# Kernel tuning notes

Hardware: AMD Instinct MI355X
Metric: run time of the kernel (lower is better)

Reference implementation:

```python
import jax, jax.numpy as jnp
import numpy as np

RHO = 1.0          # ADMM penalty
LAM = 0.1          # lambda_sparse
MAX_ITERS = 20
ZETA = 0.05        # APAS drift threshold / CDS temperature
TAU = 0.1          # chiral stabilizer tolerance
STEP = 0.1         # gradient step size
COHESION = 1.0     # Mohr-Coulomb cohesion
MU = 0.5           # Mohr-Coulomb friction coefficient
DP_K = 10.0        # Drucker-Prager deviatoric-norm radius


def _pas(c):
    # Phase Alignment Invariant: scalar phase-coherence metric in [0,1]
    return jnp.abs(jnp.mean(jnp.cos(c)))


def _chirality(c):
    # odd (sign-sensitive) global moment
    return jnp.mean(c ** 3)


def _mc_proj(c, g):
    # Mohr-Coulomb yield projection: clamp magnitude to cohesion + mu*|grad|
    return jnp.sign(c) * jnp.minimum(jnp.abs(c), COHESION + MU * jnp.abs(g))


def _dp_proj(c):
    # Drucker-Prager: project deviatoric part onto norm ball of radius DP_K (per row)
    m = jnp.mean(c, axis=-1, keepdims=True)
    dev = c - m
    n = jnp.linalg.norm(dev, axis=-1, keepdims=True)
    scale = jnp.minimum(1.0, DP_K / (n + 1e-8))
    return m + dev * scale


def setup_inputs() -> dict:
    key = jax.random.key(0)
    k1, k2, k3 = jax.random.split(key, 3)
    B, D = 1024, 2048
    initial_c = 0.5 * jax.random.normal(k1, (B, D), dtype=jnp.float32)
    W = jax.random.normal(k2, (D, D), dtype=jnp.float32) / np.float32(np.sqrt(D))
    love_w = 1.0 + 0.01 * jax.random.normal(k3, (D,), dtype=jnp.float32)
    love_b = jnp.zeros((D,), dtype=jnp.float32)
    return {"initial_c": initial_c, "W": W, "love_w": love_w, "love_b": love_b}


def _forward(initial_c, W, love_w, love_b):
    c_sym = initial_c
    c0 = initial_c
    z0 = c0
    u0 = jnp.zeros_like(c0)
    prev_pas0 = _pas(c0)
    prev_score0 = -_chirality(c0)  # drift = 0 -> exp(0) = 1

    def step(carry, _):
        c, z, u, prev_pas, prev_score, low, done = carry

        def energy(ci):
            pred = ci @ W  # forward_op_fn
            violation_pressure = 0.5 * jnp.sum((pred - ci) ** 2)
            admm_tension = 0.5 * RHO * jnp.sum((ci - z + u) ** 2)
            return violation_pressure + admm_tension

        g = jax.grad(energy)(c)
        c_yield = _mc_proj(c, g)
        c_next = (c_yield * love_w + love_b) - STEP * g  # LoveVector then step
        z_in = c_next + u
        thr = LAM / RHO
        z_next = jnp.sign(z_in) * jnp.maximum(jnp.abs(z_in) - thr, 0.0)
        u_next = u + (c_next - z_next)

        cur_pas = _pas(c_next)
        drift = jnp.abs(cur_pas - prev_pas)
        violation = drift > ZETA
        low = jnp.where(cur_pas < 0.5, low + 1, 0)
        done = done | (low > 20)
        cur_score = -_chirality(c_next) * jnp.exp(-drift / ZETA)
        stable = (cur_score - prev_score) >= -TAU
        acc = (~violation) & stable & (~done)

        sel = lambda a, b: jnp.where(acc, a, b)
        new = (sel(c_next, c), sel(z_next, z), sel(u_next, u),
               jnp.where(acc, cur_pas, prev_pas),
               jnp.where(acc, cur_score, prev_score), low, done)
        return new, None

    init = (c0, z0, u0, prev_pas0, prev_score0,
            jnp.zeros((), jnp.int32), jnp.zeros((), jnp.bool_))
    (c_phys, z, u, _, _, _, _), _ = jax.lax.scan(step, init, None, length=MAX_ITERS)

    diff = jnp.linalg.norm(c_phys - c_sym)
    chi_cur = _chirality(c_phys)
    chi_orig = _chirality(c_sym)
    status = jnp.where(jnp.sign(chi_cur) != jnp.sign(chi_orig),
                       2,
                       jnp.where(diff > 5.0, 2, jnp.where(diff > 1.0, 1, 0))).astype(jnp.int32)

    delta = c_phys - c_sym
    symbolic_delta = jnp.round(delta * 10.0) / 10.0
    c_compressed = _dp_proj(c_sym + symbolic_delta)
    return c_compressed, status


def reference(initial_c, W, love_w, love_b):
    return _forward(initial_c, W, love_w, love_b)
```

## Files before the change

### kernel.cpp

```cpp
#include <hip/hip_runtime.h>
#include <math.h>

#define D 2048
#define BROWS 1024
#define NEL (D*BROWS)
#define NBLK 1024
#define NTHREADS_TOT (NBLK*256)

#define GM 128
#define GN 128
#define GK 16

__device__ __forceinline__ double blk_reduce(double v, double* sm) {
    const int t = threadIdx.x;
    sm[t] = v;
    __syncthreads();
    for (int s = 128; s > 0; s >>= 1) {
        if (t < s) sm[t] += sm[t + s];
        __syncthreads();
    }
    double r = sm[0];
    __syncthreads();
    return r;
}

__global__ __launch_bounds__(256) void k_gemm(const float* __restrict__ A,
        const float* __restrict__ B, float* __restrict__ P0, float* __restrict__ P1,
        const float* __restrict__ Wadj, int ksz, int mode, const int* __restrict__ frz)
{
    if (frz && *frz) return;
    __shared__ float As[2][GK][GM + 4];
    __shared__ float Bs[2][GK][GN + 4];
    const int t  = threadIdx.x;
    const int tx = t & 15, ty = t >> 4;
    const int row0 = blockIdx.y * GM, col0 = blockIdx.x * GN;
    const int k0 = blockIdx.z * ksz;
    float* __restrict__ out = blockIdx.z ? P1 : P0;

    const int r0 = t >> 2, cq = t & 3;

    float acc[8][8];
    #pragma unroll
    for (int i = 0; i < 8; ++i)
        #pragma unroll
        for (int j = 0; j < 8; ++j) acc[i][j] = 0.0f;

    const int ntiles = ksz / GK;
    float4 rga[2], rgb[2];

    #pragma unroll
    for (int v = 0; v < 2; ++v) {
        rga[v] = *reinterpret_cast<const float4*>(&A[(size_t)(row0 + r0 + 64*v) * D + k0 + cq*4]);
        rgb[v] = *reinterpret_cast<const float4*>(&B[(size_t)(col0 + r0 + 64*v) * D + k0 + cq*4]);
    }
    #pragma unroll
    for (int v = 0; v < 2; ++v) {
        As[0][cq*4+0][r0+64*v] = rga[v].x; As[0][cq*4+1][r0+64*v] = rga[v].y;
        As[0][cq*4+2][r0+64*v] = rga[v].z; As[0][cq*4+3][r0+64*v] = rga[v].w;
        Bs[0][cq*4+0][r0+64*v] = rgb[v].x; Bs[0][cq*4+1][r0+64*v] = rgb[v].y;
        Bs[0][cq*4+2][r0+64*v] = rgb[v].z; Bs[0][cq*4+3][r0+64*v] = rgb[v].w;
    }
    __syncthreads();

    for (int tt = 0; tt < ntiles; ++tt) {
        const int cur = tt & 1;
        if (tt + 1 < ntiles) {
            const int kb = k0 + (tt + 1) * GK;
            #pragma unroll
            for (int v = 0; v < 2; ++v) {
                rga[v] = *reinterpret_cast<const float4*>(&A[(size_t)(row0 + r0 + 64*v) * D + kb + cq*4]);
                rgb[v] = *reinterpret_cast<const float4*>(&B[(size_t)(col0 + r0 + 64*v) * D + kb + cq*4]);
            }
        }
        #pragma unroll
        for (int k = 0; k < GK; ++k) {
            float a[8], b[8];
            *reinterpret_cast<float4*>(&a[0]) = *reinterpret_cast<const float4*>(&As[cur][k][ty*4]);
            *reinterpret_cast<float4*>(&a[4]) = *reinterpret_cast<const float4*>(&As[cur][k][64 + ty*4]);
            *reinterpret_cast<float4*>(&b[0]) = *reinterpret_cast<const float4*>(&Bs[cur][k][tx*4]);
            *reinterpret_cast<float4*>(&b[4]) = *reinterpret_cast<const float4*>(&Bs[cur][k][64 + tx*4]);
            #pragma unroll
            for (int i = 0; i < 8; ++i)
                #pragma unroll
                for (int j = 0; j < 8; ++j)
                    acc[i][j] += a[i] * b[j];
        }
        if (tt + 1 < ntiles) {
            const int nb = cur ^ 1;
            __syncthreads();
            #pragma unroll
            for (int v = 0; v < 2; ++v) {
                As[nb][cq*4+0][r0+64*v] = rga[v].x; As[nb][cq*4+1][r0+64*v] = rga[v].y;
                As[nb][cq*4+2][r0+64*v] = rga[v].z; As[nb][cq*4+3][r0+64*v] = rga[v].w;
                Bs[nb][cq*4+0][r0+64*v] = rgb[v].x; Bs[nb][cq*4+1][r0+64*v] = rgb[v].y;
                Bs[nb][cq*4+2][r0+64*v] = rgb[v].z; Bs[nb][cq*4+3][r0+64*v] = rgb[v].w;
            }
            __syncthreads();
        }
    }

    #pragma unroll
    for (int i = 0; i < 8; ++i) {
        const int grow = row0 + ((i < 4) ? (ty*4 + i) : (64 + ty*4 + i - 4));
        float vv[8];
        #pragma unroll
        for (int j = 0; j < 8; ++j) vv[j] = acc[i][j];
        if (mode == 0) {
            #pragma unroll
            for (int j = 0; j < 8; ++j) {
                const int gcol = col0 + ((j < 4) ? (tx*4 + j) : (64 + tx*4 + j - 4));
                const float wsum = Wadj[(size_t)grow * D + gcol] + Wadj[(size_t)gcol * D + grow];
                vv[j] += (grow == gcol ? 1.0f : 0.0f) - wsum;
            }
        }
        float* orow = &out[(size_t)grow * D + col0];
        *reinterpret_cast<float4*>(&orow[tx*4]) =
            make_float4(vv[0], vv[1], vv[2], vv[3]);
        *reinterpret_cast<float4*>(&orow[64 + tx*4]) =
            make_float4(vv[4], vv[5], vv[6], vv[7]);
    }
}

__global__ __launch_bounds__(256) void k_init(const float* __restrict__ c0,
        float* __restrict__ c, float* __restrict__ z, float* __restrict__ u,
        double* __restrict__ partials)
{
    __shared__ double sm[256];
    double sc = 0.0, s3 = 0.0;
    const int tid = blockIdx.x * 256 + threadIdx.x;
    const float4 zero4 = make_float4(0.f, 0.f, 0.f, 0.f);
    for (int i4 = tid; i4 < NEL/4; i4 += NTHREADS_TOT) {
        const float4 v4 = reinterpret_cast<const float4*>(c0)[i4];
        reinterpret_cast<float4*>(c)[i4] = v4;
        reinterpret_cast<float4*>(z)[i4] = v4;
        reinterpret_cast<float4*>(u)[i4] = zero4;
        const float va[4] = {v4.x, v4.y, v4.z, v4.w};
        #pragma unroll
        for (int L = 0; L < 4; ++L) {
            sc += (double)cosf(va[L]);
            s3 += (double)((va[L] * va[L]) * va[L]);
        }
    }
    const double tc = blk_reduce(sc, sm);
    const double t3 = blk_reduce(s3, sm);
    if (threadIdx.x == 0) { partials[blockIdx.x] = tc; partials[NBLK + blockIdx.x] = t3; }
}

__global__ __launch_bounds__(256) void k_decide0(const double* __restrict__ partials,
        double* __restrict__ scal, int* __restrict__ flag, int* __restrict__ frz,
        int* __restrict__ sel)
{
    __shared__ double sm[256];
    const int t = threadIdx.x;
    const double a = partials[t] + partials[t+256] + partials[t+512] + partials[t+768];
    const double b = partials[NBLK+t] + partials[NBLK+t+256] + partials[NBLK+t+512] + partials[NBLK+t+768];
    const double tc = blk_reduce(a, sm);
    const double t3 = blk_reduce(b, sm);
    if (t == 0) {
        const double pas = fabs(tc / (double)NEL);
        const double chi = t3 / (double)NEL;
        scal[0] = pas; scal[1] = -chi; scal[2] = chi;
        *flag = 0; *frz = 0; *sel = 0;
    }
}

__global__ __launch_bounds__(256) void k_elem_pp(const float* __restrict__ P0,
        const float* __restrict__ P1, const float* __restrict__ cc,
        float* __restrict__ cn, float* __restrict__ z, float* __restrict__ u,
        const float* __restrict__ lw, const float* __restrict__ lb,
        double* __restrict__ partials, const int* __restrict__ frz)
{
#pragma clang fp contract(off)
    if (*frz) return;
    __shared__ double sm[256];
    double sc = 0.0, s3 = 0.0;
    const int tid = blockIdx.x * 256 + threadIdx.x;
    for (int i4 = tid; i4 < NEL/4; i4 += NTHREADS_TOT) {
        const int j4 = i4 & (D/4 - 1);
        const float4 p0 = reinterpret_cast<const float4*>(P0)[i4];
        const float4 p1 = reinterpret_cast<const float4*>(P1)[i4];
        const float4 cv4 = reinterpret_cast<const float4*>(cc)[i4];
        const float4 zv4 = reinterpret_cast<const float4*>(z)[i4];
        const float4 uv4 = reinterpret_cast<const float4*>(u)[i4];
        const float4 w4 = reinterpret_cast<const float4*>(lw)[j4];
        const float4 b4 = reinterpret_cast<const float4*>(lb)[j4];
        const float p0a[4] = {p0.x, p0.y, p0.z, p0.w};
        const float p1a[4] = {p1.x, p1.y, p1.z, p1.w};
        const float cva[4] = {cv4.x, cv4.y, cv4.z, cv4.w};
        const float zva[4] = {zv4.x, zv4.y, zv4.z, zv4.w};
        const float uva[4] = {uv4.x, uv4.y, uv4.z, uv4.w};
        const float w4a[4] = {w4.x, w4.y, w4.z, w4.w};
        const float b4a[4] = {b4.x, b4.y, b4.z, b4.w};
        float Rc[4], Rz[4], Ru[4];
        #pragma unroll
        for (int L = 0; L < 4; ++L) {
            const float cv = cva[L];
            const float uv = uva[L];
            const float g = (p0a[L] + p1a[L]) + ((cv - zva[L]) + uv);
            const float lim = 1.0f + 0.5f * fabsf(g);
            const float mn = fminf(fabsf(cv), lim);
            const float cy = (cv > 0.0f) ? mn : ((cv < 0.0f) ? -mn : 0.0f);
            const float cnv = (cy * w4a[L] + b4a[L]) - 0.1f * g;
            Rc[L] = cnv;
            const float zi = cnv + uv;
            float zm = fabsf(zi) - 0.1f;
            zm = fmaxf(zm, 0.0f);
            const float zn = (zi > 0.0f) ? zm : ((zi < 0.0f) ? -zm : 0.0f);
            Rz[L] = zn;
            Ru[L] = uv + (cnv - zn);
            sc += (double)cosf(cnv);
            s3 += (double)((cnv * cnv) * cnv);
        }
        reinterpret_cast<float4*>(cn)[i4] = make_float4(Rc[0], Rc[1], Rc[2], Rc[3]);
        reinterpret_cast<float4*>(z)[i4]  = make_float4(Rz[0], Rz[1], Rz[2], Rz[3]);
        reinterpret_cast<float4*>(u)[i4]  = make_float4(Ru[0], Ru[1], Ru[2], Ru[3]);
    }
    const double tc = blk_reduce(sc, sm);
    const double t3 = blk_reduce(s3, sm);
    if (threadIdx.x == 0) { partials[blockIdx.x] = tc; partials[NBLK + blockIdx.x] = t3; }
}

__global__ __launch_bounds__(256) void k_elem(float* __restrict__ P0,
        const float* __restrict__ P1, const float* __restrict__ c,
        const float* __restrict__ z, const float* __restrict__ u,
        const float* __restrict__ lw, const float* __restrict__ lb,
        double* __restrict__ partials, const int* __restrict__ frz)
{
#pragma clang fp contract(off)
    if (*frz) return;
    __shared__ double sm[256];
    double sc = 0.0, s3 = 0.0;
    const int tid = blockIdx.x * 256 + threadIdx.x;
    for (int i = tid; i < NEL; i += NTHREADS_TOT) {
        const int j = i & (D - 1);
        const float cv = c[i];
        const float g = (P0[i] + P1[i]) + ((cv - z[i]) + u[i]);
        const float lim = 1.0f + 0.5f * fabsf(g);
        const float mn = fminf(fabsf(cv), lim);
        const float cy = (cv > 0.0f) ? mn : ((cv < 0.0f) ? -mn : 0.0f);
        const float cnv = (cy * lw[j] + lb[j]) - 0.1f * g;
        P0[i] = cnv;
        sc += (double)cosf(cnv);
        s3 += (double)((cnv * cnv) * cnv);
    }
    const double tc = blk_reduce(sc, sm);
    const double t3 = blk_reduce(s3, sm);
    if (threadIdx.x == 0) { partials[blockIdx.x] = tc; partials[NBLK + blockIdx.x] = t3; }
}

__global__ __launch_bounds__(256) void k_decide(const double* __restrict__ partials,
        double* __restrict__ scal, int* __restrict__ flag, int* __restrict__ frz,
        int* __restrict__ sel, int next_sel)
{
    __shared__ double sm[256];
    if (*frz) return;
    const int t = threadIdx.x;
    const double a = partials[t] + partials[t+256] + partials[t+512] + partials[t+768];
    const double b = partials[NBLK+t] + partials[NBLK+t+256] + partials[NBLK+t+512] + partials[NBLK+t+768];
    const double tc = blk_reduce(a, sm);
    const double t3 = blk_reduce(b, sm);
    if (t == 0) {
        const double pas = fabs(tc / (double)NEL);
        const double drift = fabs(pas - scal[0]);
        const double chi = t3 / (double)NEL;
        const double score = -chi * exp(-drift / 0.05);
        const bool violation = drift > 0.05;
        const bool stable = (score - scal[1]) >= -0.1;
        const int acc = (!violation && stable) ? 1 : 0;
        *flag = acc;
        if (acc) { scal[0] = pas; scal[1] = score; *sel = next_sel; }
        else     { *frz = 1; }
    }
}

__global__ __launch_bounds__(256) void k_commit(const float* __restrict__ cn,
        float* __restrict__ c, float* __restrict__ z, float* __restrict__ u,
        const int* __restrict__ flag)
{
#pragma clang fp contract(off)
    if (*flag == 0) return;
    const int tid = blockIdx.x * 256 + threadIdx.x;
    for (int i = tid; i < NEL; i += NTHREADS_TOT) {
        const float cnv = cn[i];
        const float uv = u[i];
        const float zi = cnv + uv;
        float zm = fabsf(zi) - 0.1f;
        zm = fmaxf(zm, 0.0f);
        const float zn = (zi > 0.0f) ? zm : ((zi < 0.0f) ? -zm : 0.0f);
        c[i] = cnv;
        z[i] = zn;
        u[i] = uv + (cnv - zn);
    }
}

__global__ __launch_bounds__(256) void k_final_rows(const float* __restrict__ c0,
        const float* __restrict__ cA, const float* __restrict__ cB,
        const int* __restrict__ sel, float* __restrict__ outp)
{
#pragma clang fp contract(off)
    __shared__ double sm[256];
    const float* __restrict__ c = (*sel) ? cB : cA;
    const int row = blockIdx.x;
    const size_t base = (size_t)row * D;
    float tv[8];
    double s1 = 0.0;
    #pragma unroll
    for (int s = 0; s < 8; ++s) {
        const int j = threadIdx.x + s * 256;
        const float s0 = c0[base + j];
        const float delta = c[base + j] - s0;
        const float sym = rintf(delta * 10.0f) / 10.0f;
        const float tval = s0 + sym;
        tv[s] = tval;
        s1 += (double)tval;
    }
    const double tot = blk_reduce(s1, sm);
    const float m = (float)(tot / (double)D);
    double s2 = 0.0;
    #pragma unroll
    for (int s = 0; s < 8; ++s) {
        const float dev = tv[s] - m;
        s2 += (double)(dev * dev);
    }
    const double tot2 = blk_reduce(s2, sm);
    const float n = sqrtf((float)tot2);
    const float scale = fminf(1.0f, 10.0f / (n + 1e-8f));
    #pragma unroll
    for (int s = 0; s < 8; ++s) {
        const int j = threadIdx.x + s * 256;
        outp[base + j] = m + (tv[s] - m) * scale;
    }
}

__global__ __launch_bounds__(256) void k_final_glob(const float* __restrict__ c0,
        const float* __restrict__ cA, const float* __restrict__ cB,
        const int* __restrict__ sel, double* __restrict__ partials)
{
    __shared__ double sm[256];
    const float* __restrict__ c = (*sel) ? cB : cA;
    double s3 = 0.0, sd = 0.0;
    const int tid = blockIdx.x * 256 + threadIdx.x;
    for (int i = tid; i < NEL; i += NTHREADS_TOT) {
        const float v = c[i];
        s3 += (double)((v * v) * v);
        const float d = v - c0[i];
        sd += (double)(d * d);
    }
    const double t3 = blk_reduce(s3, sm);
    const double td = blk_reduce(sd, sm);
    if (threadIdx.x == 0) { partials[blockIdx.x] = t3; partials[NBLK + blockIdx.x] = td; }
}

__global__ __launch_bounds__(256) void k_final_status(const double* __restrict__ partials,
        const double* __restrict__ scal, float* __restrict__ outp)
{
    __shared__ double sm[256];
    const int t = threadIdx.x;
    const double a = partials[t] + partials[t+256] + partials[t+512] + partials[t+768];
    const double b = partials[NBLK+t] + partials[NBLK+t+256] + partials[NBLK+t+512] + partials[NBLK+t+768];
    const double t3 = blk_reduce(a, sm);
    const double td = blk_reduce(b, sm);
    if (t == 0) {
        const double chi_cur = t3 / (double)NEL;
        const double diff = sqrt(td);
        const double chi_orig = scal[2];
        const int s_cur = (chi_cur > 0.0) - (chi_cur < 0.0);
        const int s_org = (chi_orig > 0.0) - (chi_orig < 0.0);
        int status;
        if (s_cur != s_org)   status = 2;
        else if (diff > 5.0)  status = 2;
        else if (diff > 1.0)  status = 1;
        else                  status = 0;
        outp[NEL] = (float)status;
    }
}

extern "C" void kernel_launch(void* const* d_in, const int* in_sizes, int n_in,
                              void* d_out, int out_size, void* d_ws, size_t ws_size,
                              hipStream_t stream)
{
    const float* c0 = (const float*)d_in[0];
    const float* W  = (const float*)d_in[1];
    const float* lw = (const float*)d_in[2];
    const float* lb = (const float*)d_in[3];
    float* outp = (float*)d_out;

    const size_t M4 = (size_t)D * D;
    const size_t N4 = (size_t)NEL;
    float* Mb = (float*)d_ws;
    float* region = Mb + M4;

    const size_t tail_bytes = (2 * NBLK + 8) * sizeof(double) + 4 * sizeof(int);
    const bool pp = ws_size >= (M4 + 6 * N4) * sizeof(float) + tail_bytes;

    float *cA, *cB, *z, *u, *P0, *P1;
    if (pp) { cA = region; cB = cA + N4; z = cB + N4; u = z + N4; P0 = u + N4; P1 = P0 + N4; }
    else    { cA = region; cB = cA;      z = cA + N4; u = z + N4; P0 = u + N4; P1 = P0 + N4; }
    double* partials = (double*)(P1 + N4);
    double* scal = partials + 2 * NBLK;
    int* flag = (int*)(scal + 8);
    int* frz  = flag + 1;
    int* sel  = frz + 1;

    k_gemm<<<dim3(D / GN, D / GM, 1), 256, 0, stream>>>(W, W, Mb, Mb, W, D, 0, nullptr);
    k_init<<<NBLK, 256, 0, stream>>>(c0, cA, z, u, partials);
    k_decide0<<<1, 256, 0, stream>>>(partials, scal, flag, frz, sel);

    for (int t = 0; t < 20; ++t) {
        const float* ccur = (pp && (t & 1)) ? cB : cA;
        float* cnxt = (pp && !(t & 1)) ? cB : cA;
        k_gemm<<<dim3(D / GN, BROWS / GM, 2), 256, 0, stream>>>(ccur, Mb, P0, P1, nullptr, D / 2, 1, frz);
        if (pp) {
            k_elem_pp<<<NBLK, 256, 0, stream>>>(P0, P1, ccur, cnxt, z, u, lw, lb, partials, frz);
            k_decide<<<1, 256, 0, stream>>>(partials, scal, flag, frz, sel, (t + 1) & 1);
        } else {
            k_elem<<<NBLK, 256, 0, stream>>>(P0, P1, cA, z, u, lw, lb, partials, frz);
            k_decide<<<1, 256, 0, stream>>>(partials, scal, flag, frz, sel, 0);
            k_commit<<<NBLK, 256, 0, stream>>>(P0, cA, z, u, flag);
        }
    }

    k_final_rows<<<BROWS, 256, 0, stream>>>(c0, cA, cB, sel, outp);
    k_final_glob<<<NBLK, 256, 0, stream>>>(c0, cA, cB, sel, partials);
    k_final_status<<<1, 256, 0, stream>>>(partials, scal, outp);
}
```

Baseline: 3.541 ms.

## Shrink GEMM tile to 64x128, deepen K tile, add XCD-aware block mapping

Changes the SGEMM tile from 128x128x16 with register-prefetch double buffering to 64x128x32 with single-buffered shared memory. The grid becomes 1D with a block-index remap that keeps same-row tiles on one XCD, aiming for better L2 reuse. Grid size doubles from 256 to 512 blocks, so 256 CUs get better occupancy and wave balance. In exchange the kernel has lower arithmetic intensity per thread and loses the global-load/compute overlap of double buffering.

```diff
diff --git a/kernel.cpp b/kernel.cpp
--- a/kernel.cpp
+++ b/kernel.cpp
@@ -7,9 +7,9 @@
 #define NBLK 1024
 #define NTHREADS_TOT (NBLK*256)
 
-#define GM 128
+#define GM 64
 #define GN 128
-#define GK 16
+#define GK 32
 
 __device__ __forceinline__ double blk_reduce(double v, double* sm) {
     const int t = threadIdx.x;
@@ -26,82 +26,72 @@
 
 __global__ __launch_bounds__(256) void k_gemm(const float* __restrict__ A,
         const float* __restrict__ B, float* __restrict__ P0, float* __restrict__ P1,
-        const float* __restrict__ Wadj, int ksz, int mode, const int* __restrict__ frz)
+        const float* __restrict__ Wadj, int ksz, int mode, const int* __restrict__ frz,
+        int nx, int ypg)
 {
     if (frz && *frz) return;
-    __shared__ float As[2][GK][GM + 4];
-    __shared__ float Bs[2][GK][GN + 4];
+    __shared__ float As[GK][GM + 4];
+    __shared__ float Bs[GK][GN + 4];
     const int t  = threadIdx.x;
     const int tx = t & 15, ty = t >> 4;
-    const int row0 = blockIdx.y * GM, col0 = blockIdx.x * GN;
-    const int k0 = blockIdx.z * ksz;
-    float* __restrict__ out = blockIdx.z ? P1 : P0;
-
-    const int r0 = t >> 2, cq = t & 3;
-
-    float acc[8][8];
+
+    const int wg  = blockIdx.x;
+    const int xcd = wg & 7;
+    const int idx = wg >> 3;
+    const int y   = xcd + 8 * (idx % ypg);
+    const int tmp = idx / ypg;
+    const int x   = tmp % nx;
+    const int zz  = tmp / nx;
+
+    const int row0 = y * GM, col0 = x * GN;
+    const int k0 = zz * ksz;
+    float* __restrict__ out = zz ? P1 : P0;
+
+    float acc[4][8];
     #pragma unroll
-    for (int i = 0; i < 8; ++i)
+    for (int i = 0; i < 4; ++i)
         #pragma unroll
         for (int j = 0; j < 8; ++j) acc[i][j] = 0.0f;
 
-    const int ntiles = ksz / GK;
-    float4 rga[2], rgb[2];
-
-    #pragma unroll
-    for (int v = 0; v < 2; ++v) {
-        rga[v] = *reinterpret_cast<const float4*>(&A[(size_t)(row0 + r0 + 64*v) * D + k0 + cq*4]);
-        rgb[v] = *reinterpret_cast<const float4*>(&B[(size_t)(col0 + r0 + 64*v) * D + k0 + cq*4]);
-    }
-    #pragma unroll
-    for (int v = 0; v < 2; ++v) {
-        As[0][cq*4+0][r0+64*v] = rga[v].x; As[0][cq*4+1][r0+64*v] = rga[v].y;
-        As[0][cq*4+2][r0+64*v] = rga[v].z; As[0][cq*4+3][r0+64*v] = rga[v].w;
-        Bs[0][cq*4+0][r0+64*v] = rgb[v].x; Bs[0][cq*4+1][r0+64*v] = rgb[v].y;
-        Bs[0][cq*4+2][r0+64*v] = rgb[v].z; Bs[0][cq*4+3][r0+64*v] = rgb[v].w;
-    }
-    __syncthreads();
-
-    for (int tt = 0; tt < ntiles; ++tt) {
-        const int cur = tt & 1;
-        if (tt + 1 < ntiles) {
-            const int kb = k0 + (tt + 1) * GK;
+    for (int kt = 0; kt < ksz; kt += GK) {
+        const int kb = k0 + kt;
+        #pragma unroll
+        for (int v = 0; v < 2; ++v) {
+            const int vid = t + v * 256;
+            const int r = vid >> 3, q = vid & 7;
+            const float4 ga = *reinterpret_cast<const float4*>(
+                &A[(size_t)(row0 + r) * D + kb + q * 4]);
+            As[q*4+0][r] = ga.x; As[q*4+1][r] = ga.y;
+            As[q*4+2][r] = ga.z; As[q*4+3][r] = ga.w;
+        }
+        #pragma unroll
+        for (int v = 0; v < 4; ++v) {
+            const int vid = t + v * 256;
+            const int r = vid >> 3, q = vid & 7;
+            const float4 gb = *reinterpret_cast<const float4*>(
+                &B[(size_t)(col0 + r) * D + kb + q * 4]);
+            Bs[q*4+0][r] = gb.x; Bs[q*4+1][r] = gb.y;
+            Bs[q*4+2][r] = gb.z; Bs[q*4+3][r] = gb.w;
+        }
+        __syncthreads();
+        #pragma unroll
+        for (int k = 0; k < GK; ++k) {
+            float a[4], b[8];
+            *reinterpret_cast<float4*>(&a[0]) = *reinterpret_cast<const float4*>(&As[k][ty*4]);
+            *reinterpret_cast<float4*>(&b[0]) = *reinterpret_cast<const float4*>(&Bs[k][tx*4]);
+            *reinterpret_cast<float4*>(&b[4]) = *reinterpret_cast<const float4*>(&Bs[k][64 + tx*4]);
             #pragma unroll
-            for (int v = 0; v < 2; ++v) {
-                rga[v] = *reinterpret_cast<const float4*>(&A[(size_t)(row0 + r0 + 64*v) * D + kb + cq*4]);
-                rgb[v] = *reinterpret_cast<const float4*>(&B[(size_t)(col0 + r0 + 64*v) * D + kb + cq*4]);
-            }
-        }
-        #pragma unroll
-        for (int k = 0; k < GK; ++k) {
-            float a[8], b[8];
-            *reinterpret_cast<float4*>(&a[0]) = *reinterpret_cast<const float4*>(&As[cur][k][ty*4]);
-            *reinterpret_cast<float4*>(&a[4]) = *reinterpret_cast<const float4*>(&As[cur][k][64 + ty*4]);
-            *reinterpret_cast<float4*>(&b[0]) = *reinterpret_cast<const float4*>(&Bs[cur][k][tx*4]);
-            *reinterpret_cast<float4*>(&b[4]) = *reinterpret_cast<const float4*>(&Bs[cur][k][64 + tx*4]);
-            #pragma unroll
-            for (int i = 0; i < 8; ++i)
+            for (int i = 0; i < 4; ++i)
                 #pragma unroll
                 for (int j = 0; j < 8; ++j)
                     acc[i][j] += a[i] * b[j];
         }
-        if (tt + 1 < ntiles) {
-            const int nb = cur ^ 1;
-            __syncthreads();
-            #pragma unroll
-            for (int v = 0; v < 2; ++v) {
-                As[nb][cq*4+0][r0+64*v] = rga[v].x; As[nb][cq*4+1][r0+64*v] = rga[v].y;
-                As[nb][cq*4+2][r0+64*v] = rga[v].z; As[nb][cq*4+3][r0+64*v] = rga[v].w;
-                Bs[nb][cq*4+0][r0+64*v] = rgb[v].x; Bs[nb][cq*4+1][r0+64*v] = rgb[v].y;
-                Bs[nb][cq*4+2][r0+64*v] = rgb[v].z; Bs[nb][cq*4+3][r0+64*v] = rgb[v].w;
-            }
-            __syncthreads();
-        }
+        __syncthreads();
     }
 
     #pragma unroll
-    for (int i = 0; i < 8; ++i) {
-        const int grow = row0 + ((i < 4) ? (ty*4 + i) : (64 + ty*4 + i - 4));
+    for (int i = 0; i < 4; ++i) {
+        const int grow = row0 + ty*4 + i;
         float vv[8];
         #pragma unroll
         for (int j = 0; j < 8; ++j) vv[j] = acc[i][j];
@@ -402,14 +392,14 @@
     int* frz  = flag + 1;
     int* sel  = frz + 1;
 
-    k_gemm<<<dim3(D / GN, D / GM, 1), 256, 0, stream>>>(W, W, Mb, Mb, W, D, 0, nullptr);
+    k_gemm<<<512, 256, 0, stream>>>(W, W, Mb, Mb, W, D, 0, nullptr, 16, 4);
     k_init<<<NBLK, 256, 0, stream>>>(c0, cA, z, u, partials);
     k_decide0<<<1, 256, 0, stream>>>(partials, scal, flag, frz, sel);
 
     for (int t = 0; t < 20; ++t) {
         const float* ccur = (pp && (t & 1)) ? cB : cA;
         float* cnxt = (pp && !(t & 1)) ? cB : cA;
-        k_gemm<<<dim3(D / GN, BROWS / GM, 2), 256, 0, stream>>>(ccur, Mb, P0, P1, nullptr, D / 2, 1, frz);
+        k_gemm<<<512, 256, 0, stream>>>(ccur, Mb, P0, P1, nullptr, D / 2, 1, frz, 16, 2);
         if (pp) {
             k_elem_pp<<<NBLK, 256, 0, stream>>>(P0, P1, ccur, cnxt, z, u, lw, lb, partials, frz);
             k_decide<<<1, 256, 0, stream>>>(partials, scal, flag, frz, sel, (t + 1) & 1);
```

After: 3.071 ms. 1.15x faster.

## Shrink GEMM tile to 64x128 and restructure double-buffered K loop

Applied to the files above, without the earlier changes.

Halves the GEMM row tile from 128 to 64 so each thread accumulates a 4x8 block, and adds a min-blocks-per-SM launch bound of 2 to raise occupancy. The K loop is unrolled by two with static buffer indices and precomputed pointers, replacing per-iteration index arithmetic. The intent is more blocks in flight and fewer registers per thread, hiding memory latency better. The cost is lower arithmetic intensity per thread, more LDS traffic per FMA, and a loop that assumes an even tile count.

```diff
diff --git a/kernel.cpp b/kernel.cpp
--- a/kernel.cpp
+++ b/kernel.cpp
@@ -7,7 +7,7 @@
 #define NBLK 1024
 #define NTHREADS_TOT (NBLK*256)
 
-#define GM 128
+#define GM 64
 #define GN 128
 #define GK 16
 
@@ -24,7 +24,7 @@
     return r;
 }
 
-__global__ __launch_bounds__(256) void k_gemm(const float* __restrict__ A,
+__global__ __launch_bounds__(256, 2) void k_gemm(const float* __restrict__ A,
         const float* __restrict__ B, float* __restrict__ P0, float* __restrict__ P1,
         const float* __restrict__ Wadj, int ksz, int mode, const int* __restrict__ frz)
 {
@@ -37,71 +37,74 @@
     const int k0 = blockIdx.z * ksz;
     float* __restrict__ out = blockIdx.z ? P1 : P0;
 
-    const int r0 = t >> 2, cq = t & 3;
-
-    float acc[8][8];
+    const int wr = t >> 2, wq = t & 3;
+    const float* pA  = A + (size_t)(row0 + wr) * D + (k0 + wq * 4);
+    const float* pB0 = B + (size_t)(col0 + wr) * D + (k0 + wq * 4);
+    const float* pB1 = B + (size_t)(col0 + 64 + wr) * D + (k0 + wq * 4);
+
+    float acc[4][8];
     #pragma unroll
-    for (int i = 0; i < 8; ++i)
+    for (int i = 0; i < 4; ++i)
         #pragma unroll
         for (int j = 0; j < 8; ++j) acc[i][j] = 0.0f;
 
     const int ntiles = ksz / GK;
-    float4 rga[2], rgb[2];
+    float4 ga, gb0, gb1;
+
+#define LOADR { \
+    ga  = *reinterpret_cast<const float4*>(pA);  \
+    gb0 = *reinterpret_cast<const float4*>(pB0); \
+    gb1 = *reinterpret_cast<const float4*>(pB1); \
+    pA += GK; pB0 += GK; pB1 += GK; }
+
+#define STAGE(BUF) { \
+    As[BUF][wq*4+0][wr] = ga.x;  As[BUF][wq*4+1][wr] = ga.y;  \
+    As[BUF][wq*4+2][wr] = ga.z;  As[BUF][wq*4+3][wr] = ga.w;  \
+    Bs[BUF][wq*4+0][wr] = gb0.x; Bs[BUF][wq*4+1][wr] = gb0.y; \
+    Bs[BUF][wq*4+2][wr] = gb0.z; Bs[BUF][wq*4+3][wr] = gb0.w; \
+    Bs[BUF][wq*4+0][wr+64] = gb1.x; Bs[BUF][wq*4+1][wr+64] = gb1.y; \
+    Bs[BUF][wq*4+2][wr+64] = gb1.z; Bs[BUF][wq*4+3][wr+64] = gb1.w; }
+
+#define COMPUTE(BUF) { \
+    _Pragma("unroll") \
+    for (int k = 0; k < GK; ++k) { \
+        float a[4], b[8]; \
+        *reinterpret_cast<float4*>(&a[0]) = *reinterpret_cast<const float4*>(&As[BUF][k][ty*4]); \
+        *reinterpret_cast<float4*>(&b[0]) = *reinterpret_cast<const float4*>(&Bs[BUF][k][tx*4]); \
+        *reinterpret_cast<float4*>(&b[4]) = *reinterpret_cast<const float4*>(&Bs[BUF][k][64 + tx*4]); \
+        _Pragma("unroll") \
+        for (int i = 0; i < 4; ++i) \
+            _Pragma("unroll") \
+            for (int j = 0; j < 8; ++j) \
+                acc[i][j] += a[i] * b[j]; \
+    } }
+
+    LOADR;
+    STAGE(0);
+    __syncthreads();
+
+    for (int tt = 0; tt < ntiles; tt += 2) {
+        LOADR;
+        COMPUTE(0);
+        STAGE(1);
+        __syncthreads();
+        if (tt + 2 < ntiles) {
+            LOADR;
+            COMPUTE(1);
+            STAGE(0);
+            __syncthreads();
+        } else {
+            COMPUTE(1);
+        }
+    }
+
+#undef LOADR
+#undef STAGE
+#undef COMPUTE
 
     #pragma unroll
-    for (int v = 0; v < 2; ++v) {
-        rga[v] = *reinterpret_cast<const float4*>(&A[(size_t)(row0 + r0 + 64*v) * D + k0 + cq*4]);
-        rgb[v] = *reinterpret_cast<const float4*>(&B[(size_t)(col0 + r0 + 64*v) * D + k0 + cq*4]);
-    }
-    #pragma unroll
-    for (int v = 0; v < 2; ++v) {
-        As[0][cq*4+0][r0+64*v] = rga[v].x; As[0][cq*4+1][r0+64*v] = rga[v].y;
-        As[0][cq*4+2][r0+64*v] = rga[v].z; As[0][cq*4+3][r0+64*v] = rga[v].w;
-        Bs[0][cq*4+0][r0+64*v] = rgb[v].x; Bs[0][cq*4+1][r0+64*v] = rgb[v].y;
-        Bs[0][cq*4+2][r0+64*v] = rgb[v].z; Bs[0][cq*4+3][r0+64*v] = rgb[v].w;
-    }
-    __syncthreads();
-
-    for (int tt = 0; tt < ntiles; ++tt) {
-        const int cur = tt & 1;
-        if (tt + 1 < ntiles) {
-            const int kb = k0 + (tt + 1) * GK;
-            #pragma unroll
-            for (int v = 0; v < 2; ++v) {
-                rga[v] = *reinterpret_cast<const float4*>(&A[(size_t)(row0 + r0 + 64*v) * D + kb + cq*4]);
-                rgb[v] = *reinterpret_cast<const float4*>(&B[(size_t)(col0 + r0 + 64*v) * D + kb + cq*4]);
-            }
-        }
-        #pragma unroll
-        for (int k = 0; k < GK; ++k) {
-            float a[8], b[8];
-            *reinterpret_cast<float4*>(&a[0]) = *reinterpret_cast<const float4*>(&As[cur][k][ty*4]);
-            *reinterpret_cast<float4*>(&a[4]) = *reinterpret_cast<const float4*>(&As[cur][k][64 + ty*4]);
-            *reinterpret_cast<float4*>(&b[0]) = *reinterpret_cast<const float4*>(&Bs[cur][k][tx*4]);
-            *reinterpret_cast<float4*>(&b[4]) = *reinterpret_cast<const float4*>(&Bs[cur][k][64 + tx*4]);
-            #pragma unroll
-            for (int i = 0; i < 8; ++i)
-                #pragma unroll
-                for (int j = 0; j < 8; ++j)
-                    acc[i][j] += a[i] * b[j];
-        }
-        if (tt + 1 < ntiles) {
-            const int nb = cur ^ 1;
-            __syncthreads();
-            #pragma unroll
-            for (int v = 0; v < 2; ++v) {
-                As[nb][cq*4+0][r0+64*v] = rga[v].x; As[nb][cq*4+1][r0+64*v] = rga[v].y;
-                As[nb][cq*4+2][r0+64*v] = rga[v].z; As[nb][cq*4+3][r0+64*v] = rga[v].w;
-                Bs[nb][cq*4+0][r0+64*v] = rgb[v].x; Bs[nb][cq*4+1][r0+64*v] = rgb[v].y;
-                Bs[nb][cq*4+2][r0+64*v] = rgb[v].z; Bs[nb][cq*4+3][r0+64*v] = rgb[v].w;
-            }
-            __syncthreads();
-        }
-    }
-
-    #pragma unroll
-    for (int i = 0; i < 8; ++i) {
-        const int grow = row0 + ((i < 4) ? (ty*4 + i) : (64 + ty*4 + i - 4));
+    for (int i = 0; i < 4; ++i) {
+        const int grow = row0 + ty*4 + i;
         float vv[8];
         #pragma unroll
         for (int j = 0; j < 8; ++j) vv[j] = acc[i][j];
```

Measured after the change: 2.856 ms. 19.3% less time.
